# Kernel tuning notes

Measured on AMD Instinct MI355X. Metric: run time of the kernel, lower is better.

The kernel has to match this reference:

```python
import jax, jax.numpy as jnp
import numpy as np

B, N, T, D = 8, 512, 64, 128
H = 8
DK = D // H
KS = 3
CAUSAL_PAD = KS - 1          # query conv: pad both sides, crop tail
SYM_PAD = (KS - 1) // 2      # key conv: 'same' padding


def setup_inputs() -> dict:
    key0 = jax.random.key(0)
    ks = jax.random.split(key0, 12)
    s = 0.05  # weight scale to keep activations in a sane range
    inp = {
        "query": jax.random.normal(ks[0], (B, N, T, D), jnp.float32),
        "key": jax.random.normal(ks[1], (B, N, T, D), jnp.float32),
        "value": jax.random.normal(ks[2], (B, N, T, D), jnp.float32),
        # causal mask (batch, T, T): 1 where attention allowed
        "mask": jnp.broadcast_to(jnp.tril(jnp.ones((T, T), jnp.int32)), (B, T, T)),
        "Wq": jax.random.normal(ks[3], (D, D, 1, KS), jnp.float32) * s,
        "bq": jax.random.normal(ks[4], (D,), jnp.float32) * s,
        "Wk": jax.random.normal(ks[5], (D, D, 1, KS), jnp.float32) * s,
        "bk": jax.random.normal(ks[6], (D,), jnp.float32) * s,
        "W0": jax.random.normal(ks[7], (D, D), jnp.float32) * s,
        "b0": jax.random.normal(ks[8], (D,), jnp.float32) * s,
        "W1": jax.random.normal(ks[9], (D, D), jnp.float32) * s,
        "b1": jax.random.normal(ks[10], (D,), jnp.float32) * s,
        "query_multi_segment": 0,
        "key_multi_segment": 1,
    }
    return inp


def _temporal_conv(x, W, b, pad):
    # x: (B, N, T, D) -> NCHW (B, D, N, T); W: (O, I, 1, K) OIHW
    xt = jnp.transpose(x, (0, 3, 1, 2))
    y = jax.lax.conv_general_dilated(
        xt, W, window_strides=(1, 1),
        padding=[(0, 0), (pad, pad)],
        dimension_numbers=("NCHW", "OIHW", "NCHW"))
    return y + b[None, :, None, None]  # (B, D, N, T')


def _to_heads(y_bdnt, nbatches):
    # (B, D, N, T) -> view (B, H, DK, N, T) -> permute -> (B, N, H, T, DK)
    Bb, Dd, Nn, Tt = y_bdnt.shape
    y = y_bdnt.reshape(Bb, H, DK, Nn, Tt)
    return jnp.transpose(y, (0, 3, 1, 4, 2))


def reference(query, key, value, mask, Wq, bq, Wk, bk, W0, b0, W1, b1,
              query_multi_segment, key_multi_segment):
    del query_multi_segment, key_multi_segment  # static: (False, True) branch, h_length == T
    nbatches = query.shape[0]

    # causal conv for query: pad (k-1) both sides, crop last (k-1)
    q = _temporal_conv(query, Wq, bq, CAUSAL_PAD)[:, :, :, :-CAUSAL_PAD]
    q = _to_heads(q, nbatches)                       # (B, N, H, T, DK)
    # 'same' conv for key
    k = _to_heads(_temporal_conv(key, Wk, bk, SYM_PAD), nbatches)  # (B, N, H, T, DK)

    # value linear: x @ W0.T + b0, then split heads
    v = jnp.einsum("bntd,ed->bnte", value, W0) + b0
    v = jnp.transpose(v.reshape(nbatches, N, T, H, DK), (0, 1, 3, 2, 4))  # (B, N, H, T, DK)

    scores = jnp.einsum("bnhqd,bnhkd->bnhqk", q, k) / jnp.sqrt(jnp.float32(DK))
    m = mask[:, None, None, :, :]                    # (B, 1, 1, T, T)
    scores = jnp.where(m == 0, jnp.float32(-1e9), scores)
    p_attn = jax.nn.softmax(scores, axis=-1)         # dropout p=0.0 -> identity

    x = jnp.einsum("bnhqk,bnhkd->bnhqd", p_attn, v)  # (B, N, H, T, DK)
    x = jnp.transpose(x, (0, 1, 3, 2, 4)).reshape(nbatches, N, T, H * DK)
    return jnp.einsum("bntd,ed->bnte", x, W1) + b1
```

## Files before the change

### kernel.cpp

```cpp
#include <hip/hip_runtime.h>
#include <hip/hip_bf16.h>
#include <stdint.h>

constexpr int Tt = 64;
constexpr int Dd = 128;
constexpr int BN = 4096;

typedef short s16x8 __attribute__((ext_vector_type(8)));
typedef short s16x4 __attribute__((ext_vector_type(4)));
typedef float f32x4 __attribute__((ext_vector_type(4)));

__device__ __forceinline__ short f2bf(float f) {
  return (short)__bfloat16_as_ushort(__float2bfloat16(f));
}

#define SQ_OFF   0
#define SK_OFF   17408
#define SV_OFF   34816
#define SP_OFF   51200
#define LDS_TOTAL 67584

__device__ __forceinline__ int swz256(int row, int colElem) {
  return (row << 8) + ((colElem << 1) ^ ((row & 7) << 4));
}
__device__ __forceinline__ int swz128(int row, int colElem) {
  return (row << 7) + ((colElem << 1) ^ ((row & 7) << 4));
}
__device__ __forceinline__ int swzP(int row, int colElem) {
  return (row << 7) + (((colElem << 1) ^ ((row & 7) << 4)) ^ ((row & 8) << 2));
}

__global__ void prep_weights(const float* __restrict__ Wq, const float* __restrict__ Wk,
                             const float* __restrict__ W0, const float* __restrict__ W1,
                             short* __restrict__ ws) {
  int i = blockIdx.x * 256 + threadIdx.x;
  if (i >= 131072) return;
  if (i < 49152) {
    int s = i >> 14, rem = i & 16383, o = rem >> 7, ii = rem & 127;
    ws[i] = f2bf(Wq[(o * 128 + ii) * 3 + s]);
  } else if (i < 98304) {
    int j = i - 49152;
    int s = j >> 14, rem = j & 16383, o = rem >> 7, ii = rem & 127;
    ws[i] = f2bf(Wk[(o * 128 + ii) * 3 + s]);
  } else if (i < 114688) {
    ws[i] = f2bf(W0[i - 98304]);
  } else {
    ws[i] = f2bf(W1[i - 114688]);
  }
}

__launch_bounds__(512, 4)
__global__ void fused_attn(const float* __restrict__ query, const float* __restrict__ key,
                           const float* __restrict__ value, const short* __restrict__ wsb,
                           const float* __restrict__ bq, const float* __restrict__ bk,
                           const float* __restrict__ b0, const float* __restrict__ b1,
                           float* __restrict__ out) {
  __shared__ unsigned char smem[LDS_TOTAL];
  const int bn = blockIdx.x;
  const int tid = threadIdx.x;
  const int wave = tid >> 6;
  const int lane = tid & 63;
  const size_t base = (size_t)bn * (Tt * Dd);

  const int cb = wave;
  const int col = cb * 16 + (lane & 15);
  const int ke = 8 * (lane >> 4);
  const int arow = lane & 15;

  if (tid < 128) {
    int bufOff = (tid >= 64) ? SK_OFF : SQ_OFF;
    int ri = (tid >> 4) & 3;
    int row = (ri < 2) ? ri : 64 + ri;
    s16x8 z = {};
    *(s16x8*)(smem + bufOff + swz256(row, (tid & 15) * 8)) = z;
  }
  {
#pragma unroll
    for (int t3 = 0; t3 < 3; ++t3) {
      const float* sp = (t3 == 0) ? query : (t3 == 1) ? key : value;
      const float4* s4 = (const float4*)(sp + base);
      const int off = (t3 == 0) ? SQ_OFF : (t3 == 1) ? SK_OFF : SV_OFF;
      const int rshift = (t3 == 2) ? 0 : 2;
      for (int i = tid; i < 2048; i += 512) {
        float4 v = s4[i];
        int row = (i >> 5) + rshift, c4 = (i & 31) << 2;
        s16x4 b = {f2bf(v.x), f2bf(v.y), f2bf(v.z), f2bf(v.w)};
        *(s16x4*)(smem + off + swz256(row, c4)) = b;
      }
    }
  }
  __syncthreads();

  f32x4 aq[4], ak[4], av[4];
#pragma unroll
  for (int rb = 0; rb < 4; ++rb) {
    aq[rb] = (f32x4){0.f, 0.f, 0.f, 0.f};
    ak[rb] = (f32x4){0.f, 0.f, 0.f, 0.f};
    av[rb] = (f32x4){0.f, 0.f, 0.f, 0.f};
  }
  const short* wq = wsb;
  const short* wk = wsb + 49152;
  const short* wv = wsb + 98304;
  const short* w1 = wsb + 114688;

#pragma unroll
  for (int s = 0; s < 3; ++s) {
    s16x8 bq8[4], bk8[4];
#pragma unroll
    for (int kk = 0; kk < 4; ++kk) {
      bq8[kk] = *(const s16x8*)(wq + (s << 14) + (col << 7) + kk * 32 + ke);
      bk8[kk] = *(const s16x8*)(wk + (s << 14) + (col << 7) + kk * 32 + ke);
    }
#pragma unroll
    for (int kk = 0; kk < 4; ++kk) {
#pragma unroll
      for (int rb = 0; rb < 4; ++rb) {
        s16x8 afq = *(const s16x8*)(smem + SQ_OFF + swz256(rb * 16 + arow + s, kk * 32 + ke));
        aq[rb] = __builtin_amdgcn_mfma_f32_16x16x32_bf16(afq, bq8[kk], aq[rb], 0, 0, 0);
        s16x8 afk = *(const s16x8*)(smem + SK_OFF + swz256(rb * 16 + arow + s + 1, kk * 32 + ke));
        ak[rb] = __builtin_amdgcn_mfma_f32_16x16x32_bf16(afk, bk8[kk], ak[rb], 0, 0, 0);
      }
    }
  }
  {
    s16x8 bv8[4];
#pragma unroll
    for (int kk = 0; kk < 4; ++kk)
      bv8[kk] = *(const s16x8*)(wv + (col << 7) + kk * 32 + ke);
#pragma unroll
    for (int kk = 0; kk < 4; ++kk) {
#pragma unroll
      for (int rb = 0; rb < 4; ++rb) {
        s16x8 afv = *(const s16x8*)(smem + SV_OFF + swz256(rb * 16 + arow, kk * 32 + ke));
        av[rb] = __builtin_amdgcn_mfma_f32_16x16x32_bf16(afv, bv8[kk], av[rb], 0, 0, 0);
      }
    }
  }
  __syncthreads();

  {
    const float bqv = bq[col], bkv = bk[col], b0v = b0[col];
#pragma unroll
    for (int rb = 0; rb < 4; ++rb) {
#pragma unroll
      for (int r = 0; r < 4; ++r) {
        const int row = rb * 16 + (lane >> 4) * 4 + r;
        *(short*)(smem + SQ_OFF + swz256(row, col)) = f2bf(aq[rb][r] + bqv);
        *(short*)(smem + SK_OFF + swz256(row, col)) = f2bf(ak[rb][r] + bkv);
        *(short*)(smem + SV_OFF + swz128(col, row)) = f2bf(av[rb][r] + b0v);
      }
    }
  }
  s16x8 w1f[4];
#pragma unroll
  for (int kk = 0; kk < 4; ++kk)
    w1f[kk] = *(const s16x8*)(w1 + (col << 7) + kk * 32 + ke);
  __syncthreads();

  {
    const int rb = wave & 3, hh = wave >> 2;
    const int sel = lane >> 5;
    const int aRow = sel ? 66 : (rb * 16 + arow);
    int bRow[4];
#pragma unroll
    for (int c = 0; c < 4; ++c) bRow[c] = sel ? 66 : (c * 16 + arow);
    unsigned char* sp = smem + SP_OFF + wave * 2048;
#pragma unroll
    for (int hi = 0; hi < 4; ++hi) {
      const int h = hh * 4 + hi;
      f32x4 sacc[4];
#pragma unroll
      for (int c = 0; c < 4; ++c) sacc[c] = (f32x4){0.f, 0.f, 0.f, 0.f};
      s16x8 af = *(const s16x8*)(smem + SQ_OFF + swz256(aRow, h * 16 + ke));
#pragma unroll
      for (int c = 0; c < 4; ++c) {
        s16x8 bf = *(const s16x8*)(smem + SK_OFF + swz256(bRow[c], h * 16 + ke));
        sacc[c] = __builtin_amdgcn_mfma_f32_16x16x32_bf16(af, bf, sacc[c], 0, 0, 0);
      }
      const int r0 = rb * 16 + (lane >> 4) * 4;
      float p[4][4], mx[4], sm[4];
#pragma unroll
      for (int r = 0; r < 4; ++r) mx[r] = -3.0e38f;
#pragma unroll
      for (int c = 0; c < 4; ++c) {
        const int scol = c * 16 + (lane & 15);
#pragma unroll
        for (int r = 0; r < 4; ++r) {
          float sv = (scol <= r0 + r) ? sacc[c][r] * 0.25f : -3.0e38f;
          p[c][r] = sv;
          mx[r] = fmaxf(mx[r], sv);
        }
      }
#pragma unroll
      for (int off = 1; off < 16; off <<= 1) {
#pragma unroll
        for (int r = 0; r < 4; ++r) mx[r] = fmaxf(mx[r], __shfl_xor(mx[r], off));
      }
#pragma unroll
      for (int r = 0; r < 4; ++r) sm[r] = 0.f;
#pragma unroll
      for (int c = 0; c < 4; ++c) {
#pragma unroll
        for (int r = 0; r < 4; ++r) {
          float e = __expf(p[c][r] - mx[r]);
          p[c][r] = e;
          sm[r] += e;
        }
      }
#pragma unroll
      for (int off = 1; off < 16; off <<= 1) {
#pragma unroll
        for (int r = 0; r < 4; ++r) sm[r] += __shfl_xor(sm[r], off);
      }
      float inv[4];
#pragma unroll
      for (int r = 0; r < 4; ++r) inv[r] = 1.0f / sm[r];
#pragma unroll
      for (int c = 0; c < 4; ++c) {
#pragma unroll
        for (int r = 0; r < 4; ++r)
          *(short*)(sp + swzP((lane >> 4) * 4 + r, c * 16 + (lane & 15))) = f2bf(p[c][r]);
      }
      asm volatile("s_waitcnt lgkmcnt(0)" ::: "memory");
      f32x4 xacc = (f32x4){0.f, 0.f, 0.f, 0.f};
#pragma unroll
      for (int kc = 0; kc < 2; ++kc) {
        s16x8 pf = *(const s16x8*)(sp + swzP(arow, kc * 32 + ke));
        s16x8 vf = *(const s16x8*)(smem + SV_OFF + swz128(h * 16 + arow, kc * 32 + ke));
        xacc = __builtin_amdgcn_mfma_f32_16x16x32_bf16(pf, vf, xacc, 0, 0, 0);
      }
#pragma unroll
      for (int r = 0; r < 4; ++r)
        *(short*)(smem + SQ_OFF + swz256(rb * 16 + (lane >> 4) * 4 + r, h * 16 + (lane & 15))) =
            f2bf(xacc[r] * inv[r]);
      asm volatile("s_waitcnt lgkmcnt(0)" ::: "memory");
    }
  }
  __syncthreads();

  {
    f32x4 oacc[4];
#pragma unroll
    for (int rb = 0; rb < 4; ++rb) oacc[rb] = (f32x4){0.f, 0.f, 0.f, 0.f};
#pragma unroll
    for (int kk = 0; kk < 4; ++kk) {
#pragma unroll
      for (int rb = 0; rb < 4; ++rb) {
        s16x8 af = *(const s16x8*)(smem + SQ_OFF + swz256(rb * 16 + arow, kk * 32 + ke));
        oacc[rb] = __builtin_amdgcn_mfma_f32_16x16x32_bf16(af, w1f[kk], oacc[rb], 0, 0, 0);
      }
    }
    const float bv = b1[col];
#pragma unroll
    for (int rb = 0; rb < 4; ++rb)
#pragma unroll
      for (int r = 0; r < 4; ++r) {
        const int row = rb * 16 + (lane >> 4) * 4 + r;
        out[base + (size_t)row * Dd + col] = oacc[rb][r] + bv;
      }
  }
}

extern "C" void kernel_launch(void* const* d_in, const int* in_sizes, int n_in,
                              void* d_out, int out_size, void* d_ws, size_t ws_size,
                              hipStream_t stream) {
  (void)in_sizes; (void)n_in; (void)out_size; (void)ws_size;
  const float* query = (const float*)d_in[0];
  const float* key   = (const float*)d_in[1];
  const float* value = (const float*)d_in[2];
  const float* Wq = (const float*)d_in[4];
  const float* bq = (const float*)d_in[5];
  const float* Wk = (const float*)d_in[6];
  const float* bk = (const float*)d_in[7];
  const float* W0 = (const float*)d_in[8];
  const float* b0 = (const float*)d_in[9];
  const float* W1 = (const float*)d_in[10];
  const float* b1 = (const float*)d_in[11];
  float* out = (float*)d_out;
  short* wsb = (short*)d_ws;

  hipLaunchKernelGGL(prep_weights, dim3(512), dim3(256), 0, stream, Wq, Wk, W0, W1, wsb);
  hipLaunchKernelGGL(fused_attn, dim3(BN), dim3(512), 0, stream,
                     query, key, value, wsb, bq, bk, b0, b1, out);
}
```

Before: 242.0 us.

## Keep softmax probabilities in registers via transposed score MFMA, drop P LDS buffer

Computes scores as K·Q^T so each lane holds one query row's probabilities. The softmax reduction then needs only two cross-lane shuffles, and the probabilities feed a 16x16x16 MFMA straight from registers. This removes the per-wave P scratch region in LDS, its stores and reloads, and the explicit waitcnts. With the smaller LDS footprint, the occupancy hint is raised to 6 blocks and weight-fragment loads are moved into the loops to cut register pressure, which risks more repeated global loads.

```diff
diff --git a/kernel.cpp b/kernel.cpp
--- a/kernel.cpp
+++ b/kernel.cpp
@@ -17,17 +17,13 @@
 #define SQ_OFF   0
 #define SK_OFF   17408
 #define SV_OFF   34816
-#define SP_OFF   51200
-#define LDS_TOTAL 67584
+#define LDS_TOTAL 51200
 
 __device__ __forceinline__ int swz256(int row, int colElem) {
   return (row << 8) + ((colElem << 1) ^ ((row & 7) << 4));
 }
 __device__ __forceinline__ int swz128(int row, int colElem) {
   return (row << 7) + ((colElem << 1) ^ ((row & 7) << 4));
-}
-__device__ __forceinline__ int swzP(int row, int colElem) {
-  return (row << 7) + (((colElem << 1) ^ ((row & 7) << 4)) ^ ((row & 8) << 2));
 }
 
 __global__ void prep_weights(const float* __restrict__ Wq, const float* __restrict__ Wk,
@@ -49,7 +45,7 @@
   }
 }
 
-__launch_bounds__(512, 4)
+__launch_bounds__(512, 6)
 __global__ void fused_attn(const float* __restrict__ query, const float* __restrict__ key,
                            const float* __restrict__ value, const short* __restrict__ wsb,
                            const float* __restrict__ bq, const float* __restrict__ bk,
@@ -104,35 +100,26 @@
   const short* w1 = wsb + 114688;
 
 #pragma unroll
+  for (int kk = 0; kk < 4; ++kk) {
+    s16x8 bvf = *(const s16x8*)(wv + (col << 7) + kk * 32 + ke);
+#pragma unroll
+    for (int rb = 0; rb < 4; ++rb) {
+      s16x8 afv = *(const s16x8*)(smem + SV_OFF + swz256(rb * 16 + arow, kk * 32 + ke));
+      av[rb] = __builtin_amdgcn_mfma_f32_16x16x32_bf16(afv, bvf, av[rb], 0, 0, 0);
+    }
+  }
+#pragma unroll
   for (int s = 0; s < 3; ++s) {
-    s16x8 bq8[4], bk8[4];
 #pragma unroll
     for (int kk = 0; kk < 4; ++kk) {
-      bq8[kk] = *(const s16x8*)(wq + (s << 14) + (col << 7) + kk * 32 + ke);
-      bk8[kk] = *(const s16x8*)(wk + (s << 14) + (col << 7) + kk * 32 + ke);
-    }
-#pragma unroll
-    for (int kk = 0; kk < 4; ++kk) {
+      s16x8 bqf = *(const s16x8*)(wq + (s << 14) + (col << 7) + kk * 32 + ke);
+      s16x8 bkf = *(const s16x8*)(wk + (s << 14) + (col << 7) + kk * 32 + ke);
 #pragma unroll
       for (int rb = 0; rb < 4; ++rb) {
         s16x8 afq = *(const s16x8*)(smem + SQ_OFF + swz256(rb * 16 + arow + s, kk * 32 + ke));
-        aq[rb] = __builtin_amdgcn_mfma_f32_16x16x32_bf16(afq, bq8[kk], aq[rb], 0, 0, 0);
+        aq[rb] = __builtin_amdgcn_mfma_f32_16x16x32_bf16(afq, bqf, aq[rb], 0, 0, 0);
         s16x8 afk = *(const s16x8*)(smem + SK_OFF + swz256(rb * 16 + arow + s + 1, kk * 32 + ke));
-        ak[rb] = __builtin_amdgcn_mfma_f32_16x16x32_bf16(afk, bk8[kk], ak[rb], 0, 0, 0);
-      }
-    }
-  }
-  {
-    s16x8 bv8[4];
-#pragma unroll
-    for (int kk = 0; kk < 4; ++kk)
-      bv8[kk] = *(const s16x8*)(wv + (col << 7) + kk * 32 + ke);
-#pragma unroll
-    for (int kk = 0; kk < 4; ++kk) {
-#pragma unroll
-      for (int rb = 0; rb < 4; ++rb) {
-        s16x8 afv = *(const s16x8*)(smem + SV_OFF + swz256(rb * 16 + arow, kk * 32 + ke));
-        av[rb] = __builtin_amdgcn_mfma_f32_16x16x32_bf16(afv, bv8[kk], av[rb], 0, 0, 0);
+        ak[rb] = __builtin_amdgcn_mfma_f32_16x16x32_bf16(afk, bkf, ak[rb], 0, 0, 0);
       }
     }
   }
@@ -151,89 +138,65 @@
       }
     }
   }
-  s16x8 w1f[4];
-#pragma unroll
-  for (int kk = 0; kk < 4; ++kk)
-    w1f[kk] = *(const s16x8*)(w1 + (col << 7) + kk * 32 + ke);
   __syncthreads();
 
   {
     const int rb = wave & 3, hh = wave >> 2;
+    const int g = lane >> 4;
+    const int qrow = lane & 15;
     const int sel = lane >> 5;
-    const int aRow = sel ? 66 : (rb * 16 + arow);
-    int bRow[4];
-#pragma unroll
-    for (int c = 0; c < 4; ++c) bRow[c] = sel ? 66 : (c * 16 + arow);
-    unsigned char* sp = smem + SP_OFF + wave * 2048;
 #pragma unroll
     for (int hi = 0; hi < 4; ++hi) {
       const int h = hh * 4 + hi;
+      s16x8 bfq = *(const s16x8*)(smem + SQ_OFF + swz256(rb * 16 + qrow, h * 16 + ke));
       f32x4 sacc[4];
 #pragma unroll
-      for (int c = 0; c < 4; ++c) sacc[c] = (f32x4){0.f, 0.f, 0.f, 0.f};
-      s16x8 af = *(const s16x8*)(smem + SQ_OFF + swz256(aRow, h * 16 + ke));
-#pragma unroll
       for (int c = 0; c < 4; ++c) {
-        s16x8 bf = *(const s16x8*)(smem + SK_OFF + swz256(bRow[c], h * 16 + ke));
-        sacc[c] = __builtin_amdgcn_mfma_f32_16x16x32_bf16(af, bf, sacc[c], 0, 0, 0);
-      }
-      const int r0 = rb * 16 + (lane >> 4) * 4;
-      float p[4][4], mx[4], sm[4];
-#pragma unroll
-      for (int r = 0; r < 4; ++r) mx[r] = -3.0e38f;
+        const int kr = sel ? 66 : (c * 16 + qrow);
+        s16x8 af = *(const s16x8*)(smem + SK_OFF + swz256(kr, h * 16 + ke));
+        sacc[c] = __builtin_amdgcn_mfma_f32_16x16x32_bf16(
+            af, bfq, (f32x4){0.f, 0.f, 0.f, 0.f}, 0, 0, 0);
+      }
+      const int qg = rb * 16 + qrow;
+      float p[4][4];
+      float mx = -3.0e38f;
+#pragma unroll
+      for (int c = 0; c < 4; ++c)
+#pragma unroll
+        for (int r = 0; r < 4; ++r) {
+          const int kcol = c * 16 + 4 * g + r;
+          float sv = (kcol <= qg) ? sacc[c][r] * 0.25f : -3.0e38f;
+          p[c][r] = sv;
+          mx = fmaxf(mx, sv);
+        }
+      mx = fmaxf(mx, __shfl_xor(mx, 16));
+      mx = fmaxf(mx, __shfl_xor(mx, 32));
+      float sm = 0.f;
+#pragma unroll
+      for (int c = 0; c < 4; ++c)
+#pragma unroll
+        for (int r = 0; r < 4; ++r) {
+          float e = __expf(p[c][r] - mx);
+          p[c][r] = e;
+          sm += e;
+        }
+      sm += __shfl_xor(sm, 16);
+      sm += __shfl_xor(sm, 32);
+      const float inv = 1.0f / sm;
+      s16x4 pa[4];
+#pragma unroll
+      for (int c = 0; c < 4; ++c)
+#pragma unroll
+        for (int r = 0; r < 4; ++r) pa[c][r] = f2bf(p[c][r] * inv);
+      f32x4 xacc = (f32x4){0.f, 0.f, 0.f, 0.f};
 #pragma unroll
       for (int c = 0; c < 4; ++c) {
-        const int scol = c * 16 + (lane & 15);
-#pragma unroll
-        for (int r = 0; r < 4; ++r) {
-          float sv = (scol <= r0 + r) ? sacc[c][r] * 0.25f : -3.0e38f;
-          p[c][r] = sv;
-          mx[r] = fmaxf(mx[r], sv);
-        }
-      }
-#pragma unroll
-      for (int off = 1; off < 16; off <<= 1) {
-#pragma unroll
-        for (int r = 0; r < 4; ++r) mx[r] = fmaxf(mx[r], __shfl_xor(mx[r], off));
-      }
-#pragma unroll
-      for (int r = 0; r < 4; ++r) sm[r] = 0.f;
-#pragma unroll
-      for (int c = 0; c < 4; ++c) {
-#pragma unroll
-        for (int r = 0; r < 4; ++r) {
-          float e = __expf(p[c][r] - mx[r]);
-          p[c][r] = e;
-          sm[r] += e;
-        }
-      }
-#pragma unroll
-      for (int off = 1; off < 16; off <<= 1) {
-#pragma unroll
-        for (int r = 0; r < 4; ++r) sm[r] += __shfl_xor(sm[r], off);
-      }
-      float inv[4];
-#pragma unroll
-      for (int r = 0; r < 4; ++r) inv[r] = 1.0f / sm[r];
-#pragma unroll
-      for (int c = 0; c < 4; ++c) {
-#pragma unroll
-        for (int r = 0; r < 4; ++r)
-          *(short*)(sp + swzP((lane >> 4) * 4 + r, c * 16 + (lane & 15))) = f2bf(p[c][r]);
-      }
-      asm volatile("s_waitcnt lgkmcnt(0)" ::: "memory");
-      f32x4 xacc = (f32x4){0.f, 0.f, 0.f, 0.f};
-#pragma unroll
-      for (int kc = 0; kc < 2; ++kc) {
-        s16x8 pf = *(const s16x8*)(sp + swzP(arow, kc * 32 + ke));
-        s16x8 vf = *(const s16x8*)(smem + SV_OFF + swz128(h * 16 + arow, kc * 32 + ke));
-        xacc = __builtin_amdgcn_mfma_f32_16x16x32_bf16(pf, vf, xacc, 0, 0, 0);
+        s16x4 vf = *(const s16x4*)(smem + SV_OFF + swz128(h * 16 + qrow, c * 16 + 4 * g));
+        xacc = __builtin_amdgcn_mfma_f32_16x16x16bf16_1k(pa[c], vf, xacc, 0, 0, 0);
       }
 #pragma unroll
       for (int r = 0; r < 4; ++r)
-        *(short*)(smem + SQ_OFF + swz256(rb * 16 + (lane >> 4) * 4 + r, h * 16 + (lane & 15))) =
-            f2bf(xacc[r] * inv[r]);
-      asm volatile("s_waitcnt lgkmcnt(0)" ::: "memory");
+        *(short*)(smem + SQ_OFF + swz256(rb * 16 + 4 * g + r, h * 16 + qrow)) = f2bf(xacc[r]);
     }
   }
   __syncthreads();
@@ -244,10 +207,11 @@
     for (int rb = 0; rb < 4; ++rb) oacc[rb] = (f32x4){0.f, 0.f, 0.f, 0.f};
 #pragma unroll
     for (int kk = 0; kk < 4; ++kk) {
+      s16x8 bf = *(const s16x8*)(w1 + (col << 7) + kk * 32 + ke);
 #pragma unroll
       for (int rb = 0; rb < 4; ++rb) {
         s16x8 af = *(const s16x8*)(smem + SQ_OFF + swz256(rb * 16 + arow, kk * 32 + ke));
-        oacc[rb] = __builtin_amdgcn_mfma_f32_16x16x32_bf16(af, w1f[kk], oacc[rb], 0, 0, 0);
+        oacc[rb] = __builtin_amdgcn_mfma_f32_16x16x32_bf16(af, bf, oacc[rb], 0, 0, 0);
       }
     }
     const float bv = b1[col];
```

Measured after the change: 287.1 us. +18.6%, slower.
